# Performance work log

Hardware: AMD Instinct MI355X
Metric: run time of the kernel (lower is better)

## Reference

```python
import jax, jax.numpy as jnp
import numpy as np

N_NODES = 8192
N_EDGES = 262144
D_IN = 512
D_OUT = 512


def setup_inputs() -> dict:
    key = jax.random.key(0)
    k1, k2, k3 = jax.random.split(key, 3)
    x = jax.random.normal(k1, (N_NODES, D_IN), dtype=jnp.float32)
    edge_index = jax.random.randint(k2, (2, N_EDGES), 0, N_NODES, dtype=jnp.int64)
    weight = jax.random.normal(k3, (D_IN, D_OUT), dtype=jnp.float32)
    bias = jnp.zeros((D_OUT,), dtype=jnp.float32)
    return {"x": x, "edge_index": edge_index, "weight": weight, "bias": bias}


def reference(x, edge_index, weight, bias):
    # GCN layer with selfloop=True branch of the original module.
    n = x.shape[0]
    # Dense symmetric adjacency via scatter-set, matching adj[ei0,ei1]=1; adj[ei1,ei0]=1
    adj = jnp.zeros((n, n), dtype=x.dtype)
    adj = adj.at[edge_index[0], edge_index[1]].set(1.0)
    adj = adj.at[edge_index[1], edge_index[0]].set(1.0)
    # Add self loops, symmetric degree normalization D^{-1/2} A D^{-1/2}
    adj = adj + jnp.eye(n, dtype=x.dtype)
    deg = jnp.sum(adj, axis=1)
    dinv = 1.0 / jnp.sqrt(deg)
    adj = adj * dinv[:, None] * dinv[None, :]  # == D @ adj @ D (diagonal scaling)
    return adj @ (x @ weight) + bias
```

## Files before the change

### kernel.cpp

```cpp
#include <hip/hip_runtime.h>
#include <hip/hip_bf16.h>


#define ELL_STRIDE 128

typedef __attribute__((ext_vector_type(8))) short bf16x8;
typedef __attribute__((ext_vector_type(4))) float f32x4;

__device__ __forceinline__ unsigned short f2bf(float f) {
  unsigned u = __float_as_uint(f);
  u = (u + 0x7fff + ((u >> 16) & 1)) >> 16;
  return (unsigned short)u;
}
__device__ __forceinline__ float bflo(unsigned u) {
  return __uint_as_float(u << 16);
}
__device__ __forceinline__ float bfhi(unsigned u) {
  return __uint_as_float(u & 0xffff0000u);
}

__global__ __launch_bounds__(256) void fused_front_kernel(
    const int* __restrict__ ei, unsigned* __restrict__ mask, int n_edges,
    int words,
    const float* __restrict__ x, unsigned short* __restrict__ xb, int n4,
    const float* __restrict__ W, unsigned short* __restrict__ Wt, int K, int N,
    unsigned short* __restrict__ Hs, float* __restrict__ dinv, int n_nodes,
    int edge_blocks, int cast_blocks, int tr_blocks) {
  const int bid = blockIdx.x;
  if (bid < edge_blocks) {
    const int e = bid * 256 + threadIdx.x;
    if (e < n_edges) {
      const int u = ei[e];
      const int v = ei[e + n_edges];
      atomicOr(&mask[(size_t)u * words + (v >> 5)], 1u << (v & 31));
      atomicOr(&mask[(size_t)v * words + (u >> 5)], 1u << (u & 31));
    }
    return;
  }
  if (bid < edge_blocks + cast_blocks) {
    const int t = (bid - edge_blocks) * 256 + threadIdx.x;
    if (t < n4) {
      float4 v = ((const float4*)x)[t];
      ushort4 o;
      o.x = f2bf(v.x); o.y = f2bf(v.y); o.z = f2bf(v.z); o.w = f2bf(v.w);
      ((ushort4*)xb)[t] = o;
    }
    return;
  }
  if (bid < edge_blocks + cast_blocks + tr_blocks) {
    __shared__ float tile[32][33];
    const int b = bid - edge_blocks - cast_blocks;
    const int bx = b & ((N >> 5) - 1);
    const int by = b >> (31 - __builtin_clz(N >> 5));
    const int tx = threadIdx.x & 31;
    const int ty = threadIdx.x >> 5;
#pragma unroll
    for (int r = 0; r < 4; ++r)
      tile[ty + 8 * r][tx] = W[(size_t)(by * 32 + ty + 8 * r) * N + bx * 32 + tx];
    __syncthreads();
#pragma unroll
    for (int r = 0; r < 4; ++r)
      Wt[(size_t)(bx * 32 + ty + 8 * r) * K + by * 32 + tx] =
          f2bf(tile[tx][ty + 8 * r]);
    return;
  }
  {
    const int t = threadIdx.x;
    if (t < (N >> 1)) ((unsigned*)(Hs + (size_t)n_nodes * N))[t] = 0;
    if (t == 0) dinv[n_nodes] = 0.f;
  }
}

__global__ __launch_bounds__(256) void fused_mid_kernel(
    const unsigned short* __restrict__ xb,
    const unsigned short* __restrict__ Wt,
    unsigned short* __restrict__ Hs,
    const unsigned* __restrict__ mask, unsigned short* __restrict__ ell,
    int* __restrict__ deg, float* __restrict__ dinv,
    int M, int N, int K, int words, int gemm_blocks, int nbx_sh) {
  __shared__ unsigned short As[512 * 8];
  __shared__ unsigned short Bs[512 * 8];

  const int tid = threadIdx.x;
  const int bid = blockIdx.x;

  if (bid < gemm_blocks) {
    const int wave = tid >> 6;
    const int lane = tid & 63;
    const int q = lane >> 4;
    const int c = lane & 15;
    const int bx = bid & ((1 << nbx_sh) - 1);
    const int by = bid >> nbx_sh;
    const int m0 = by * 64;
    const int n0 = bx * 64;
    const int wr = wave >> 1, wc = wave & 1;

    f32x4 acc[2][2] = {};

    for (int k0 = 0; k0 < K; k0 += 64) {
#pragma unroll
      for (int t = 0; t < 2; ++t) {
        const int sbase = t * 256 + wave * 64;
        const int s = sbase + lane;
        const unsigned short* g =
            xb + (size_t)(m0 + (s & 63)) * K + k0 + (s >> 6) * 8;
        __builtin_amdgcn_global_load_lds(
            (const __attribute__((address_space(1))) void*)g,
            (__attribute__((address_space(3))) void*)(As + sbase * 8), 16, 0, 0);
      }
#pragma unroll
      for (int t = 0; t < 2; ++t) {
        const int sbase = t * 256 + wave * 64;
        const int s = sbase + lane;
        const int bn = s >> 3;
        const int bk = (s & 7) ^ (bn & 7);
        const unsigned short* g =
            Wt + (size_t)(n0 + bn) * K + k0 + bk * 8;
        __builtin_amdgcn_global_load_lds(
            (const __attribute__((address_space(1))) void*)g,
            (__attribute__((address_space(3))) void*)(Bs + sbase * 8), 16, 0, 0);
      }
      __syncthreads();

#pragma unroll
      for (int kk = 0; kk < 2; ++kk) {
        bf16x8 a[2], b[2];
#pragma unroll
        for (int tm = 0; tm < 2; ++tm) {
          const int row = wr * 32 + tm * 16 + c;
          a[tm] = *(const bf16x8*)(As + (((kk * 4 + q) * 64) + row) * 8);
        }
#pragma unroll
        for (int tn = 0; tn < 2; ++tn) {
          const int n = wc * 32 + tn * 16 + c;
          b[tn] = *(const bf16x8*)(Bs + (n * 8 + ((kk * 4 + q) ^ (n & 7))) * 8);
        }
#pragma unroll
        for (int tm = 0; tm < 2; ++tm)
#pragma unroll
          for (int tn = 0; tn < 2; ++tn)
            acc[tm][tn] = __builtin_amdgcn_mfma_f32_16x16x32_bf16(
                a[tm], b[tn], acc[tm][tn], 0, 0, 0);
      }
      __syncthreads();
    }

#pragma unroll
    for (int tm = 0; tm < 2; ++tm) {
#pragma unroll
      for (int r = 0; r < 4; ++r) {
        const int grow = m0 + wr * 32 + tm * 16 + q * 4 + r;
#pragma unroll
        for (int tn = 0; tn < 2; ++tn) {
          const int gcol = n0 + wc * 32 + tn * 16 + c;
          Hs[(size_t)grow * N + gcol] = f2bf(acc[tm][tn][r]);
        }
      }
    }
    return;
  }

  {
    const int wave = tid >> 6, lane = tid & 63;
    const int node = (bid - gemm_blocks) * 4 + wave;
    const unsigned* __restrict__ row = mask + (size_t)node * words;
    unsigned short* __restrict__ out = ell + (size_t)node * ELL_STRIDE;

    int running = 0;
    for (int r = 0; r < words; r += 64) {
      const int w = r + lane;
      unsigned bits = row[w];
      const int cnt = __popc(bits);
      int x = cnt;
#pragma unroll
      for (int d = 1; d < 64; d <<= 1) {
        int y = __shfl_up(x, d, 64);
        if (lane >= d) x += y;
      }
      int pos = running + x - cnt;
      while (bits) {
        const int b = __builtin_ctz(bits);
        bits &= bits - 1;
        if (pos < ELL_STRIDE) out[pos] = (unsigned short)((w << 5) + b);
        ++pos;
      }
      running += __shfl(x, 63, 64);
    }
    for (int p = running + lane; p < ELL_STRIDE; p += 64)
      out[p] = (unsigned short)(p == running ? node : M);
    if (lane == 0) {
      const int dd = running + 1;
      deg[node] = dd < ELL_STRIDE ? dd : ELL_STRIDE;
      dinv[node] = rsqrtf((float)running + 1.0f);
    }
  }
}

__global__ __launch_bounds__(256) void spmm_kernel(
    const unsigned short* __restrict__ ell, const int* __restrict__ deg,
    const float* __restrict__ dinv, const unsigned short* __restrict__ Hs,
    const float* __restrict__ bias, float* __restrict__ out, int n, int D) {
  __shared__ uint2 ji[4][ELL_STRIDE];
  const int wave = threadIdx.x >> 6, lane = threadIdx.x & 63;
  const int i = blockIdx.x * 4 + wave;
  const unsigned rowbytes = (unsigned)(D * 2);

  {
    const unsigned j0 = ell[(size_t)i * ELL_STRIDE + lane];
    const unsigned j1 = ell[(size_t)i * ELL_STRIDE + 64 + lane];
    ji[wave][lane] = make_uint2(j0 * rowbytes, __float_as_uint(dinv[j0]));
    ji[wave][64 + lane] = make_uint2(j1 * rowbytes, __float_as_uint(dinv[j1]));
  }
  const int d = deg[i];
  const float di = dinv[i];
  const int kmax = (d + 7) & ~7;

  const char* __restrict__ hb = (const char*)(Hs + lane * 8);
  float acc[8] = {0.f, 0.f, 0.f, 0.f, 0.f, 0.f, 0.f, 0.f};

#pragma unroll 8
  for (int k = 0; k < kmax; ++k) {
    const uint2 e = ji[wave][k];
    const float dj = __uint_as_float(e.y);
    const uint4 hv = *(const uint4*)(hb + e.x);
    acc[0] += dj * bflo(hv.x); acc[1] += dj * bfhi(hv.x);
    acc[2] += dj * bflo(hv.y); acc[3] += dj * bfhi(hv.y);
    acc[4] += dj * bflo(hv.z); acc[5] += dj * bfhi(hv.z);
    acc[6] += dj * bflo(hv.w); acc[7] += dj * bfhi(hv.w);
  }

  const float4 b0 = *(const float4*)(bias + lane * 8);
  const float4 b1 = *(const float4*)(bias + lane * 8 + 4);
  float* op = out + (size_t)i * D + lane * 8;
  float4 o0, o1;
  o0.x = di * acc[0] + b0.x; o0.y = di * acc[1] + b0.y;
  o0.z = di * acc[2] + b0.z; o0.w = di * acc[3] + b0.w;
  o1.x = di * acc[4] + b1.x; o1.y = di * acc[5] + b1.y;
  o1.z = di * acc[6] + b1.z; o1.w = di * acc[7] + b1.w;
  *(float4*)op = o0;
  *(float4*)(op + 4) = o1;
}

extern "C" void kernel_launch(void* const* d_in, const int* in_sizes, int n_in,
                              void* d_out, int out_size, void* d_ws, size_t ws_size,
                              hipStream_t stream) {
  const float* x    = (const float*)d_in[0];
  const int*   ei   = (const int*)d_in[1];
  const float* W    = (const float*)d_in[2];
  const float* bias = (const float*)d_in[3];
  float* out = (float*)d_out;

  const int d_out_dim = in_sizes[3];
  const int d_in_dim  = in_sizes[2] / d_out_dim;
  const int n_nodes   = in_sizes[0] / d_in_dim;
  const int n_edges   = in_sizes[1] / 2;
  const int words     = (n_nodes + 31) / 32;

  char* ws = (char*)d_ws;
  size_t off = 0;
  unsigned* mask = (unsigned*)(ws + off); off += (size_t)n_nodes * words * 4;
  int* deg       = (int*)(ws + off);      off += (size_t)n_nodes * 4;
  float* dinv    = (float*)(ws + off);    off += (size_t)(n_nodes + 1) * 4;
  unsigned short* ell = (unsigned short*)(ws + off); off += (size_t)n_nodes * ELL_STRIDE * 2;
  unsigned short* xb  = (unsigned short*)(ws + off); off += (size_t)n_nodes * d_in_dim * 2;
  unsigned short* Wt  = (unsigned short*)(ws + off); off += (size_t)d_in_dim * d_out_dim * 2;
  unsigned short* Hs  = (unsigned short*)(ws + off);
  off += (size_t)(n_nodes + 1) * d_out_dim * 2;

  hipMemsetAsync(mask, 0, (size_t)n_nodes * words * 4, stream);

  const int edge_blocks = (n_edges + 255) / 256;
  const int n4 = n_nodes * d_in_dim / 4;
  const int cast_blocks = (n4 + 255) / 256;
  const int tr_blocks = (d_in_dim / 32) * (d_out_dim / 32);
  fused_front_kernel<<<edge_blocks + cast_blocks + tr_blocks + 1, 256, 0, stream>>>(
      ei, mask, n_edges, words, x, xb, n4, W, Wt, d_in_dim, d_out_dim,
      Hs, dinv, n_nodes, edge_blocks, cast_blocks, tr_blocks);

  const int nbx = d_out_dim / 64;
  const int nbx_sh = 31 - __builtin_clz(nbx);
  const int gemm_blocks = nbx * (n_nodes / 64);
  const int ell_blocks = n_nodes / 4;
  fused_mid_kernel<<<gemm_blocks + ell_blocks, 256, 0, stream>>>(
      xb, Wt, Hs, mask, ell, deg, dinv,
      n_nodes, d_out_dim, d_in_dim, words, gemm_blocks, nbx_sh);

  spmm_kernel<<<n_nodes / 4, 256, 0, stream>>>(ell, deg, dinv, Hs, bias, out,
                                               n_nodes, d_out_dim);
}
```

Measured before the change: 160.6 us.

## Split SpMM columns into halves pinned to XCD groups for L2 locality

The SpMM kernel now launches twice as many blocks, and each one handles half of the output columns for four rows. Block IDs are remapped so that XCDs 0-3 handle the first column half and XCDs 4-7 the second. Each XCD's L2 therefore only caches half of the bf16 H matrix, which should improve hit rates on the gathered neighbor rows. The ELL index loads and output stores also become nontemporal to avoid polluting the cache. In exchange, each wave issues smaller 8-byte gathers and the ELL and dinv neighbor lookups run twice, and the mapping assumes round-robin XCD dispatch of blocks.

```diff
diff --git a/kernel.cpp b/kernel.cpp
--- a/kernel.cpp
+++ b/kernel.cpp
@@ -202,12 +202,18 @@
     const float* __restrict__ bias, float* __restrict__ out, int n, int D) {
   __shared__ uint2 ji[4][ELL_STRIDE];
   const int wave = threadIdx.x >> 6, lane = threadIdx.x & 63;
-  const int i = blockIdx.x * 4 + wave;
+  const int bid = blockIdx.x;
+  const int xcd = bid & 7;
+  const int half = xcd >> 2;
+  const int g = (bid >> 3) * 4 + (xcd & 3);
+  const int i = g * 4 + wave;
   const unsigned rowbytes = (unsigned)(D * 2);
 
   {
-    const unsigned j0 = ell[(size_t)i * ELL_STRIDE + lane];
-    const unsigned j1 = ell[(size_t)i * ELL_STRIDE + 64 + lane];
+    const unsigned j0 =
+        __builtin_nontemporal_load(ell + (size_t)i * ELL_STRIDE + lane);
+    const unsigned j1 =
+        __builtin_nontemporal_load(ell + (size_t)i * ELL_STRIDE + 64 + lane);
     ji[wave][lane] = make_uint2(j0 * rowbytes, __float_as_uint(dinv[j0]));
     ji[wave][64 + lane] = make_uint2(j1 * rowbytes, __float_as_uint(dinv[j1]));
   }
@@ -215,30 +221,24 @@
   const float di = dinv[i];
   const int kmax = (d + 7) & ~7;
 
-  const char* __restrict__ hb = (const char*)(Hs + lane * 8);
-  float acc[8] = {0.f, 0.f, 0.f, 0.f, 0.f, 0.f, 0.f, 0.f};
+  const char* __restrict__ hb = (const char*)Hs + half * D + lane * 8;
+  float acc[4] = {0.f, 0.f, 0.f, 0.f};
 
 #pragma unroll 8
   for (int k = 0; k < kmax; ++k) {
     const uint2 e = ji[wave][k];
     const float dj = __uint_as_float(e.y);
-    const uint4 hv = *(const uint4*)(hb + e.x);
+    const uint2 hv = *(const uint2*)(hb + e.x);
     acc[0] += dj * bflo(hv.x); acc[1] += dj * bfhi(hv.x);
     acc[2] += dj * bflo(hv.y); acc[3] += dj * bfhi(hv.y);
-    acc[4] += dj * bflo(hv.z); acc[5] += dj * bfhi(hv.z);
-    acc[6] += dj * bflo(hv.w); acc[7] += dj * bfhi(hv.w);
-  }
-
-  const float4 b0 = *(const float4*)(bias + lane * 8);
-  const float4 b1 = *(const float4*)(bias + lane * 8 + 4);
-  float* op = out + (size_t)i * D + lane * 8;
-  float4 o0, o1;
+  }
+
+  const int col = half * (D >> 1) + lane * 4;
+  const float4 b0 = *(const float4*)(bias + col);
+  f32x4 o0;
   o0.x = di * acc[0] + b0.x; o0.y = di * acc[1] + b0.y;
   o0.z = di * acc[2] + b0.z; o0.w = di * acc[3] + b0.w;
-  o1.x = di * acc[4] + b1.x; o1.y = di * acc[5] + b1.y;
-  o1.z = di * acc[6] + b1.z; o1.w = di * acc[7] + b1.w;
-  *(float4*)op = o0;
-  *(float4*)(op + 4) = o1;
+  __builtin_nontemporal_store(o0, (f32x4*)(out + (size_t)i * D + col));
 }
 
 extern "C" void kernel_launch(void* const* d_in, const int* in_sizes, int n_in,
@@ -285,6 +285,7 @@
       xb, Wt, Hs, mask, ell, deg, dinv,
       n_nodes, d_out_dim, d_in_dim, words, gemm_blocks, nbx_sh);
 
-  spmm_kernel<<<n_nodes / 4, 256, 0, stream>>>(ell, deg, dinv, Hs, bias, out,
+  const int spmm_blocks = 2 * (n_nodes / 4);
+  spmm_kernel<<<spmm_blocks, 256, 0, stream>>>(ell, deg, dinv, Hs, bias, out,
                                                n_nodes, d_out_dim);
 }
```

New measurement: 161.4 us. Within noise of the previous version (+0.4%).
